# Performance work log

Hardware: AMD Instinct MI355X
Metric: run time of the kernel (lower is better)

The kernel has to match this reference:

```python
import jax, jax.numpy as jnp
import numpy as np

EMBED = 1024
HEADS = 16
HEAD_DIM = EMBED // HEADS


def setup_inputs() -> dict:
    key = jax.random.key(0)
    ks = jax.random.split(key, 7)
    N, L = 2, 2048
    values = jax.random.normal(ks[0], (N, L, EMBED), dtype=jnp.float32)
    keys = jax.random.normal(ks[1], (N, L, EMBED), dtype=jnp.float32)
    queries = jax.random.normal(ks[2], (N, L, EMBED), dtype=jnp.float32)
    mask = jax.random.randint(ks[3], (N, 1, L, L), 0, 2, dtype=jnp.int32)
    s = 1.0 / np.sqrt(HEAD_DIM)
    Wv = jax.random.normal(ks[4], (HEAD_DIM, HEAD_DIM), dtype=jnp.float32) * s
    Wk = jax.random.normal(ks[5], (HEAD_DIM, HEAD_DIM), dtype=jnp.float32) * s
    Wq = jax.random.normal(ks[6], (HEAD_DIM, HEAD_DIM), dtype=jnp.float32) * s
    return {"values": values, "keys": keys, "queries": queries, "mask": mask,
            "Wv": Wv, "Wk": Wk, "Wq": Wq}


def reference(values, keys, queries, mask, Wv, Wk, Wq):
    N, Lq = queries.shape[0], queries.shape[1]
    Lk = keys.shape[1]
    # reshape to [N, L, H, D]; nn.Linear(x) = x @ W.T (shared across heads)
    v = values.reshape(N, Lk, HEADS, HEAD_DIM) @ Wv.T
    k = keys.reshape(N, Lk, HEADS, HEAD_DIM) @ Wk.T
    q = queries.reshape(N, Lq, HEADS, HEAD_DIM) @ Wq.T
    # scores scaled by sqrt(embed_size) as in the original module
    e = jnp.einsum("nqhd,nkhd->nhqk", q, k) / jnp.sqrt(jnp.float32(EMBED))
    e = jnp.where(mask == 0, jnp.float32(-1e20), e)
    attn = jax.nn.softmax(e, axis=-1)
    out = jnp.einsum("nhqk,nkhd->nqhd", attn, v)
    return out.reshape(N, Lq, HEADS * HEAD_DIM)
```

## Files before the change

### kernel.cpp

```cpp
#include <hip/hip_runtime.h>
#include <hip/hip_bf16.h>

#define LSEQ 2048
#define NB   2
#define NH   16
#define HD   64
#define NKT  32
#define QSCALE 0.04508687049285173f

typedef __attribute__((ext_vector_type(8))) __bf16 bf16x8;
typedef __attribute__((ext_vector_type(4))) __bf16 bf16x4;
typedef __attribute__((ext_vector_type(2))) __bf16 bf16x2;
typedef __attribute__((ext_vector_type(4))) float  f32x4;

__global__ __launch_bounds__(256)
void pack_mask_kernel(const int* __restrict__ mask,
                      unsigned long long* __restrict__ mbits) {
  size_t gw = ((size_t)blockIdx.x * 256 + threadIdx.x) >> 6;
  int lane = threadIdx.x & 63;
  int v = mask[gw * 64 + lane];
  unsigned long long b = __ballot(v != 0);
  if (lane == 0) mbits[gw] = b;
}

__global__ __launch_bounds__(256)
void proj_kernel(const float* __restrict__ xv, const float* __restrict__ Wv_,
                 const float* __restrict__ xk, const float* __restrict__ Wk_,
                 const float* __restrict__ xq, const float* __restrict__ Wq_,
                 __bf16* __restrict__ outv, __bf16* __restrict__ outk,
                 __bf16* __restrict__ outq) {
  __shared__ __bf16 S[16384];
  __bf16* Xh = S;
  __bf16* Xl = S + 4096;
  __bf16* Wh = S + 8192;
  __bf16* Wl = S + 12288;

  const float* x; const float* W; __bf16* out;
  if (blockIdx.z == 0)      { x = xv; W = Wv_; out = outv; }
  else if (blockIdx.z == 1) { x = xk; W = Wk_; out = outk; }
  else                      { x = xq; W = Wq_; out = outq; }
  const float osc = (blockIdx.z == 2) ? QSCALE : 1.0f;

  const int tid = threadIdx.x;
  const int bx = blockIdx.x;
  const int h  = blockIdx.y;
  const int n  = bx >> 5;
  const int l0 = (bx & 31) << 6;

  const int r  = tid >> 2;
  const int c0 = (tid & 3) << 4;
  const float* xrow = x + ((size_t)(n * LSEQ + l0) + r) * 1024 + h * 64 + c0;
  const float* wrow = W + r * 64 + c0;

#pragma unroll
  for (int hf = 0; hf < 2; ++hf) {
    int kc = c0 + hf * 8;
    int off = r * 64 + (kc ^ ((r & 7) << 3));
    float4 a = *(const float4*)(xrow + hf * 8);
    float4 b = *(const float4*)(xrow + hf * 8 + 4);
    float va[8] = {a.x, a.y, a.z, a.w, b.x, b.y, b.z, b.w};
    bf16x8 hi, lo;
#pragma unroll
    for (int j = 0; j < 8; ++j) {
      __bf16 h_ = (__bf16)va[j];
      hi[j] = h_;
      lo[j] = (__bf16)(va[j] - (float)h_);
    }
    *(bf16x8*)(Xh + off) = hi;
    *(bf16x8*)(Xl + off) = lo;

    float4 c = *(const float4*)(wrow + hf * 8);
    float4 d = *(const float4*)(wrow + hf * 8 + 4);
    float vw[8] = {c.x, c.y, c.z, c.w, d.x, d.y, d.z, d.w};
    bf16x8 whv, wlv;
#pragma unroll
    for (int j = 0; j < 8; ++j) {
      __bf16 h_ = (__bf16)vw[j];
      whv[j] = h_;
      wlv[j] = (__bf16)(vw[j] - (float)h_);
    }
    *(bf16x8*)(Wh + off) = whv;
    *(bf16x8*)(Wl + off) = wlv;
  }
  __syncthreads();

  const int wv   = tid >> 6;
  const int lane = tid & 63;
  const int l15  = lane & 15;
  const int lhi  = lane >> 4;

  bf16x8 xhf[2], xlf[2];
  const int arow = wv * 16 + l15;
#pragma unroll
  for (int ko = 0; ko < 2; ++ko) {
    int aoff = arow * 64 + ((ko * 32 + lhi * 8) ^ ((arow & 7) << 3));
    xhf[ko] = *(const bf16x8*)(Xh + aoff);
    xlf[ko] = *(const bf16x8*)(Xl + aoff);
  }

  f32x4 acc[4] = {};
#pragma unroll
  for (int cg = 0; cg < 4; ++cg) {
    int d = cg * 16 + l15;
#pragma unroll
    for (int ko = 0; ko < 2; ++ko) {
      int boff = d * 64 + ((ko * 32 + lhi * 8) ^ ((d & 7) << 3));
      bf16x8 whf = *(const bf16x8*)(Wh + boff);
      bf16x8 wlf = *(const bf16x8*)(Wl + boff);
      acc[cg] = __builtin_amdgcn_mfma_f32_16x16x32_bf16(xhf[ko], whf, acc[cg], 0, 0, 0);
      acc[cg] = __builtin_amdgcn_mfma_f32_16x16x32_bf16(xhf[ko], wlf, acc[cg], 0, 0, 0);
      acc[cg] = __builtin_amdgcn_mfma_f32_16x16x32_bf16(xlf[ko], whf, acc[cg], 0, 0, 0);
    }
  }
  __syncthreads();

  __bf16* tb = S;
#pragma unroll
  for (int cg = 0; cg < 4; ++cg)
#pragma unroll
    for (int rr = 0; rr < 4; ++rr)
      tb[(wv * 16 + lhi * 4 + rr) * 72 + cg * 16 + l15] = (__bf16)(acc[cg][rr] * osc);
  __syncthreads();

  const int tok = tid >> 2;
  const int d0  = (tid & 3) * 16;
  bf16x8 o0 = *(const bf16x8*)(tb + tok * 72 + d0);
  bf16x8 o1 = *(const bf16x8*)(tb + tok * 72 + d0 + 8);
  size_t ob = (size_t)(n * NH + h) * LSEQ + l0;
  *(bf16x8*)(out + (ob + tok) * HD + d0)     = o0;
  *(bf16x8*)(out + (ob + tok) * HD + d0 + 8) = o1;
}

__global__ __launch_bounds__(512, 4)
void attn_kernel(const __bf16* __restrict__ Qb, const __bf16* __restrict__ Kb,
                 const __bf16* __restrict__ Vb,
                 const unsigned long long* __restrict__ mbits,
                 float* __restrict__ out) {
  __shared__ __bf16 KV[16384];
  __shared__ float  Ls[128];

  const int tid  = threadIdx.x;
  const int wid  = tid >> 6;
  const int hw   = wid >> 2;
  const int wq   = wid & 3;
  const int lane = tid & 63;
  const int l15  = lane & 15;
  const int lhi  = lane >> 4;

  const int lin = blockIdx.y * 16 + blockIdx.x;
  const int xcd = lin & 7;
  const int idx = lin >> 3;
  const int nh  = xcd + ((idx >> 4) << 3);
  const int qt  = idx & 15;
  const int n   = nh >> 4;
  const int h   = nh & 15;
  const int q0  = qt << 7;

  const __bf16* Qg = Qb + ((size_t)nh * LSEQ + q0) * HD;
  const __bf16* Kg = Kb + (size_t)nh * LSEQ * HD;
  const __bf16* Vg = Vb + (size_t)nh * LSEQ * HD;

  bf16x8 qf[2][2];
#pragma unroll
  for (int mi = 0; mi < 2; ++mi)
#pragma unroll
    for (int ks = 0; ks < 2; ++ks)
      qf[mi][ks] = *(const bf16x8*)(Qg + (size_t)(wq * 32 + mi * 16 + l15) * HD
                                       + ks * 32 + lhi * 8);

  f32x4 o[2][4] = {};
  f32x4 o_ls[2] = {};
  const unsigned long long* mrow0 =
      mbits + ((size_t)n * LSEQ + q0 + wq * 32 + l15) * NKT;
  const unsigned long long* mrow1 = mrow0 + (size_t)16 * NKT;

  bf16x8 onesf;
#pragma unroll
  for (int j = 0; j < 8; ++j) onesf[j] = (__bf16)1.0f;

  const int vkg  = lane & 15;
  const int vdgw = (wq << 2) + lhi;
  const int vslotbase = ((vkg & 8) << 2) + ((vkg & 3) << 3) + (((vkg >> 2) & 1) << 2);
  bf16x4 vv[4];

#define STAGE_K(kt_, buf_)                                                         \
  _Pragma("unroll")                                                                \
  for (int it = 0; it < 2; ++it) {                                                 \
    int chb = wq * 64 + it * 256;                                                  \
    int ch = chb + lane;                                                           \
    int skey = ch >> 3, sdc = ch & 7;                                              \
    const __bf16* src = Kg + (size_t)(kt_) * 4096 + skey * 64 + ((sdc ^ (skey & 7)) << 3); \
    __builtin_amdgcn_global_load_lds(                                              \
        (const __attribute__((address_space(1))) void*)src,                        \
        (__attribute__((address_space(3))) void*)(KV + (buf_) * 4096 + chb * 8), 16, 0, 0); \
  }
#define LOAD_V(kt_)                                                                \
  _Pragma("unroll")                                                                \
  for (int m_ = 0; m_ < 4; ++m_)                                                   \
    vv[m_] = *(const bf16x4*)(Vg + (size_t)(kt_) * 4096 + (vkg * 4 + m_) * HD + vdgw * 4);
#define WRITE_V(buf_)                                                              \
  _Pragma("unroll")                                                                \
  for (int i = 0; i < 4; ++i) {                                                    \
    int d = vdgw * 4 + i;                                                          \
    int swz = (d & 7) ^ ((d >> 3) & 7);                                            \
    bf16x4 pr; pr[0] = vv[0][i]; pr[1] = vv[1][i]; pr[2] = vv[2][i]; pr[3] = vv[3][i]; \
    *(bf16x4*)(KV + 8192 + (buf_) * 4096 + d * 64 + (vslotbase ^ (swz << 3))) = pr; \
  }

  if (hw == 1) { STAGE_K(0, 0); }
  else         { LOAD_V(0); WRITE_V(0); }
  unsigned long long w0 = mrow0[0];
  unsigned long long w1 = mrow1[0];
  __syncthreads();

  for (int kt = 0; kt < NKT; ++kt) {
    const int cur = kt & 1;
    const int nxt = cur ^ 1;
    const bool pf = (kt + 1 < NKT);
    unsigned long long nw0 = 0, nw1 = 0;
    if (pf) {
      if (hw == 1) { STAGE_K(kt + 1, nxt); }
      else         { LOAD_V(kt + 1); }
      nw0 = mrow0[kt + 1];
      nw1 = mrow1[kt + 1];
    }

    const __bf16* Kc = KV + cur * 4096;
    f32x4 s[2][2] = {};
#pragma unroll
    for (int ks = 0; ks < 2; ++ks)
#pragma unroll
      for (int t = 0; t < 2; ++t) {
        int key = hw * 32 + t * 16 + l15;
        bf16x8 kf = *(const bf16x8*)(
            Kc + key * 64 + ((ks * 32 + lhi * 8) ^ ((key & 7) << 3)));
        s[0][t] = __builtin_amdgcn_mfma_f32_16x16x32_bf16(kf, qf[0][ks], s[0][t], 0, 0, 0);
        s[1][t] = __builtin_amdgcn_mfma_f32_16x16x32_bf16(kf, qf[1][ks], s[1][t], 0, 0, 0);
      }

    bf16x8 pa[2];
#pragma unroll
    for (int mi = 0; mi < 2; ++mi) {
      unsigned long long w = mi ? w1 : w0;
      unsigned shl = (unsigned)(w >> (hw * 32 + lhi * 4));
#pragma unroll
      for (int t = 0; t < 2; ++t)
#pragma unroll
        for (int r = 0; r < 4; ++r) {
          float p = __builtin_amdgcn_exp2f(s[mi][t][r]);
          p = ((shl >> (t * 16 + r)) & 1u) ? p : 0.f;
          pa[mi][t * 4 + r] = (__bf16)p;
        }
    }

    if (hw == 0 && pf) { WRITE_V(nxt); }

    const __bf16* Vc = KV + 8192 + cur * 4096;
#pragma unroll
    for (int t = 0; t < 4; ++t) {
      int d = t * 16 + l15;
      int swz = (d & 7) ^ ((d >> 3) & 7);
      bf16x8 vf = *(const bf16x8*)(
          Vc + d * 64 + ((hw * 32 + lhi * 8) ^ (swz << 3)));
      o[0][t] = __builtin_amdgcn_mfma_f32_16x16x32_bf16(pa[0], vf, o[0][t], 0, 0, 0);
      o[1][t] = __builtin_amdgcn_mfma_f32_16x16x32_bf16(pa[1], vf, o[1][t], 0, 0, 0);
    }
    o_ls[0] = __builtin_amdgcn_mfma_f32_16x16x32_bf16(pa[0], onesf, o_ls[0], 0, 0, 0);
    o_ls[1] = __builtin_amdgcn_mfma_f32_16x16x32_bf16(pa[1], onesf, o_ls[1], 0, 0, 0);

    w0 = nw0;
    w1 = nw1;
    __syncthreads();
  }

  float* Sf = (float*)KV;
  if (hw == 1) {
#pragma unroll
    for (int mi = 0; mi < 2; ++mi) {
#pragma unroll
      for (int t = 0; t < 4; ++t)
        *(f32x4*)&Sf[wq * 2048 + (mi * 4 + t) * 256 + lane * 4] = o[mi][t];
      if (l15 == 0)
        *(f32x4*)&Ls[wq * 32 + mi * 16 + lhi * 4] = o_ls[mi];
    }
  }
  __syncthreads();
  if (hw == 0) {
#pragma unroll
    for (int mi = 0; mi < 2; ++mi) {
      f32x4 pls = *(const f32x4*)&Ls[wq * 32 + mi * 16 + lhi * 4];
      float inv[4];
#pragma unroll
      for (int r = 0; r < 4; ++r)
        inv[r] = 1.f / (o_ls[mi][r] + pls[r]);
#pragma unroll
      for (int t = 0; t < 4; ++t) {
        f32x4 po = *(const f32x4*)&Sf[wq * 2048 + (mi * 4 + t) * 256 + lane * 4];
#pragma unroll
        for (int r = 0; r < 4; ++r) {
          size_t ob = ((size_t)n * LSEQ + q0 + wq * 32 + mi * 16 + lhi * 4 + r) * 1024
                    + h * 64 + t * 16 + l15;
          out[ob] = (o[mi][t][r] + po[r]) * inv[r];
        }
      }
    }
  }
#undef STAGE_K
#undef LOAD_V
#undef WRITE_V
}

extern "C" void kernel_launch(void* const* d_in, const int* in_sizes, int n_in,
                              void* d_out, int out_size, void* d_ws, size_t ws_size,
                              hipStream_t stream) {
  const float* xv   = (const float*)d_in[0];
  const float* xk   = (const float*)d_in[1];
  const float* xq   = (const float*)d_in[2];
  const int*   mask = (const int*)d_in[3];
  const float* Wv   = (const float*)d_in[4];
  const float* Wk   = (const float*)d_in[5];
  const float* Wq   = (const float*)d_in[6];
  float* out = (float*)d_out;

  const size_t elems = (size_t)NB * NH * LSEQ * HD;
  __bf16* Qw = (__bf16*)d_ws;
  __bf16* Kw = Qw + elems;
  __bf16* Vw = Kw + elems;
  unsigned long long* mb = (unsigned long long*)(Vw + elems);

  pack_mask_kernel<<<dim3(NB * LSEQ * NKT / 4), 256, 0, stream>>>(mask, mb);
  proj_kernel<<<dim3(64, NH, 3), 256, 0, stream>>>(xv, Wv, xk, Wk, xq, Wq,
                                                   Vw, Kw, Qw);
  attn_kernel<<<dim3(16, 32), 512, 0, stream>>>(Qw, Kw, Vw, mb, out);
}
```

Baseline: 103.1 us.

## Process two key tiles per barrier with four-deep K/V LDS buffering

Restructures the attention main loop so that each synchronization period computes two key tiles and prefetches the next two into a four-slot LDS ring, doubling shared memory for K and V. This halves the number of block-wide barriers and deepens the prefetch distance, which should hide more global-load latency. The cost is twice the LDS use (64KB plus), which may cut occupancy below the launch bound's four blocks per CU, plus extra registers for the second V staging buffer.

Result: slower. 251.0 us (+143.4%).

```diff
diff --git a/kernel.cpp b/kernel.cpp
--- a/kernel.cpp
+++ b/kernel.cpp
@@ -136,7 +136,7 @@
                  const __bf16* __restrict__ Vb,
                  const unsigned long long* __restrict__ mbits,
                  float* __restrict__ out) {
-  __shared__ __bf16 KV[16384];
+  __shared__ __bf16 KV[32768];
   __shared__ float  Ls[128];
 
   const int tid  = threadIdx.x;
@@ -181,7 +181,7 @@
   const int vkg  = lane & 15;
   const int vdgw = (wq << 2) + lhi;
   const int vslotbase = ((vkg & 8) << 2) + ((vkg & 3) << 3) + (((vkg >> 2) & 1) << 2);
-  bf16x4 vv[4];
+  bf16x4 vvA[4], vvB[4];
 
 #define STAGE_K(kt_, buf_)                                                         \
   _Pragma("unroll")                                                                \
@@ -194,83 +194,92 @@
         (const __attribute__((address_space(1))) void*)src,                        \
         (__attribute__((address_space(3))) void*)(KV + (buf_) * 4096 + chb * 8), 16, 0, 0); \
   }
-#define LOAD_V(kt_)                                                                \
+#define LOAD_V(kt_, vv_)                                                           \
   _Pragma("unroll")                                                                \
   for (int m_ = 0; m_ < 4; ++m_)                                                   \
-    vv[m_] = *(const bf16x4*)(Vg + (size_t)(kt_) * 4096 + (vkg * 4 + m_) * HD + vdgw * 4);
-#define WRITE_V(buf_)                                                              \
+    vv_[m_] = *(const bf16x4*)(Vg + (size_t)(kt_) * 4096 + (vkg * 4 + m_) * HD + vdgw * 4);
+#define WRITE_V(buf_, vv_)                                                         \
   _Pragma("unroll")                                                                \
   for (int i = 0; i < 4; ++i) {                                                    \
     int d = vdgw * 4 + i;                                                          \
     int swz = (d & 7) ^ ((d >> 3) & 7);                                            \
-    bf16x4 pr; pr[0] = vv[0][i]; pr[1] = vv[1][i]; pr[2] = vv[2][i]; pr[3] = vv[3][i]; \
-    *(bf16x4*)(KV + 8192 + (buf_) * 4096 + d * 64 + (vslotbase ^ (swz << 3))) = pr; \
-  }
-
-  if (hw == 1) { STAGE_K(0, 0); }
-  else         { LOAD_V(0); WRITE_V(0); }
-  unsigned long long w0 = mrow0[0];
-  unsigned long long w1 = mrow1[0];
-  __syncthreads();
-
-  for (int kt = 0; kt < NKT; ++kt) {
-    const int cur = kt & 1;
-    const int nxt = cur ^ 1;
-    const bool pf = (kt + 1 < NKT);
-    unsigned long long nw0 = 0, nw1 = 0;
-    if (pf) {
-      if (hw == 1) { STAGE_K(kt + 1, nxt); }
-      else         { LOAD_V(kt + 1); }
-      nw0 = mrow0[kt + 1];
-      nw1 = mrow1[kt + 1];
-    }
-
-    const __bf16* Kc = KV + cur * 4096;
-    f32x4 s[2][2] = {};
-#pragma unroll
-    for (int ks = 0; ks < 2; ++ks)
-#pragma unroll
-      for (int t = 0; t < 2; ++t) {
-        int key = hw * 32 + t * 16 + l15;
-        bf16x8 kf = *(const bf16x8*)(
-            Kc + key * 64 + ((ks * 32 + lhi * 8) ^ ((key & 7) << 3)));
-        s[0][t] = __builtin_amdgcn_mfma_f32_16x16x32_bf16(kf, qf[0][ks], s[0][t], 0, 0, 0);
-        s[1][t] = __builtin_amdgcn_mfma_f32_16x16x32_bf16(kf, qf[1][ks], s[1][t], 0, 0, 0);
-      }
-
-    bf16x8 pa[2];
-#pragma unroll
-    for (int mi = 0; mi < 2; ++mi) {
-      unsigned long long w = mi ? w1 : w0;
-      unsigned shl = (unsigned)(w >> (hw * 32 + lhi * 4));
-#pragma unroll
-      for (int t = 0; t < 2; ++t)
-#pragma unroll
-        for (int r = 0; r < 4; ++r) {
-          float p = __builtin_amdgcn_exp2f(s[mi][t][r]);
-          p = ((shl >> (t * 16 + r)) & 1u) ? p : 0.f;
-          pa[mi][t * 4 + r] = (__bf16)p;
-        }
-    }
-
-    if (hw == 0 && pf) { WRITE_V(nxt); }
-
-    const __bf16* Vc = KV + 8192 + cur * 4096;
-#pragma unroll
-    for (int t = 0; t < 4; ++t) {
-      int d = t * 16 + l15;
-      int swz = (d & 7) ^ ((d >> 3) & 7);
-      bf16x8 vf = *(const bf16x8*)(
-          Vc + d * 64 + ((hw * 32 + lhi * 8) ^ (swz << 3)));
-      o[0][t] = __builtin_amdgcn_mfma_f32_16x16x32_bf16(pa[0], vf, o[0][t], 0, 0, 0);
-      o[1][t] = __builtin_amdgcn_mfma_f32_16x16x32_bf16(pa[1], vf, o[1][t], 0, 0, 0);
-    }
-    o_ls[0] = __builtin_amdgcn_mfma_f32_16x16x32_bf16(pa[0], onesf, o_ls[0], 0, 0, 0);
-    o_ls[1] = __builtin_amdgcn_mfma_f32_16x16x32_bf16(pa[1], onesf, o_ls[1], 0, 0, 0);
-
-    w0 = nw0;
-    w1 = nw1;
-    __syncthreads();
+    bf16x4 pr; pr[0] = vv_[0][i]; pr[1] = vv_[1][i]; pr[2] = vv_[2][i]; pr[3] = vv_[3][i]; \
+    *(bf16x4*)(KV + 16384 + (buf_) * 4096 + d * 64 + (vslotbase ^ (swz << 3))) = pr; \
+  }
+
+#define COMPUTE(W0_, W1_, cb_)                                                     \
+  {                                                                                \
+    const __bf16* Kc = KV + (cb_) * 4096;                                          \
+    f32x4 s[2][2] = {};                                                            \
+    _Pragma("unroll")                                                              \
+    for (int ks = 0; ks < 2; ++ks)                                                 \
+      _Pragma("unroll")                                                            \
+      for (int t = 0; t < 2; ++t) {                                                \
+        int key = hw * 32 + t * 16 + l15;                                          \
+        bf16x8 kf = *(const bf16x8*)(                                              \
+            Kc + key * 64 + ((ks * 32 + lhi * 8) ^ ((key & 7) << 3)));             \
+        s[0][t] = __builtin_amdgcn_mfma_f32_16x16x32_bf16(kf, qf[0][ks], s[0][t], 0, 0, 0); \
+        s[1][t] = __builtin_amdgcn_mfma_f32_16x16x32_bf16(kf, qf[1][ks], s[1][t], 0, 0, 0); \
+      }                                                                            \
+    bf16x8 pa[2];                                                                  \
+    _Pragma("unroll")                                                              \
+    for (int mi = 0; mi < 2; ++mi) {                                               \
+      unsigned long long w = mi ? (W1_) : (W0_);                                   \
+      unsigned shl = (unsigned)(w >> (hw * 32 + lhi * 4));                         \
+      _Pragma("unroll")                                                            \
+      for (int t = 0; t < 2; ++t)                                                  \
+        _Pragma("unroll")                                                          \
+        for (int r = 0; r < 4; ++r) {                                              \
+          float p = __builtin_amdgcn_exp2f(s[mi][t][r]);                           \
+          p = ((shl >> (t * 16 + r)) & 1u) ? p : 0.f;                              \
+          pa[mi][t * 4 + r] = (__bf16)p;                                           \
+        }                                                                          \
+    }                                                                              \
+    const __bf16* Vc = KV + 16384 + (cb_) * 4096;                                  \
+    _Pragma("unroll")                                                              \
+    for (int t = 0; t < 4; ++t) {                                                  \
+      int d = t * 16 + l15;                                                        \
+      int swz = (d & 7) ^ ((d >> 3) & 7);                                          \
+      bf16x8 vf = *(const bf16x8*)(                                                \
+          Vc + d * 64 + ((hw * 32 + lhi * 8) ^ (swz << 3)));                       \
+      o[0][t] = __builtin_amdgcn_mfma_f32_16x16x32_bf16(pa[0], vf, o[0][t], 0, 0, 0); \
+      o[1][t] = __builtin_amdgcn_mfma_f32_16x16x32_bf16(pa[1], vf, o[1][t], 0, 0, 0); \
+    }                                                                              \
+    o_ls[0] = __builtin_amdgcn_mfma_f32_16x16x32_bf16(pa[0], onesf, o_ls[0], 0, 0, 0); \
+    o_ls[1] = __builtin_amdgcn_mfma_f32_16x16x32_bf16(pa[1], onesf, o_ls[1], 0, 0, 0); \
+  }
+
+  unsigned long long w0a, w1a, w0b, w1b;
+  unsigned long long nw0a = 0, nw1a = 0, nw0b = 0, nw1b = 0;
+
+  if (hw == 1) { STAGE_K(0, 0); STAGE_K(1, 1); }
+  else         { LOAD_V(0, vvA); LOAD_V(1, vvB); }
+  w0a = mrow0[0]; w1a = mrow1[0];
+  w0b = mrow0[1]; w1b = mrow1[1];
+  if (hw == 0) { WRITE_V(0, vvA); WRITE_V(1, vvB); }
+  __syncthreads();
+
+#define PERIOD(t0_, ca_, cb_, na_, nb_, st_)                                       \
+  {                                                                                \
+    if (st_) {                                                                     \
+      if (hw == 1) { STAGE_K((t0_) + 2, na_); STAGE_K((t0_) + 3, nb_); }           \
+      else         { LOAD_V((t0_) + 2, vvA); LOAD_V((t0_) + 3, vvB); }             \
+      nw0a = mrow0[(t0_) + 2]; nw1a = mrow1[(t0_) + 2];                            \
+      nw0b = mrow0[(t0_) + 3]; nw1b = mrow1[(t0_) + 3];                            \
+    }                                                                              \
+    COMPUTE(w0a, w1a, ca_);                                                        \
+    if ((st_) && hw == 0) { WRITE_V(na_, vvA); }                                   \
+    COMPUTE(w0b, w1b, cb_);                                                        \
+    if ((st_) && hw == 0) { WRITE_V(nb_, vvB); }                                   \
+    w0a = nw0a; w1a = nw1a; w0b = nw0b; w1b = nw1b;                                \
+    __syncthreads();                                                               \
+  }
+
+  for (int kt4 = 0; kt4 < 8; ++kt4) {
+    const int t0 = kt4 * 4;
+    PERIOD(t0, 0, 1, 2, 3, true);
+    if (kt4 < 7) { PERIOD(t0 + 2, 2, 3, 0, 1, true); }
+    else         { PERIOD(t0 + 2, 2, 3, 0, 1, false); }
   }
 
   float* Sf = (float*)KV;
@@ -308,6 +317,8 @@
 #undef STAGE_K
 #undef LOAD_V
 #undef WRITE_V
+#undef COMPUTE
+#undef PERIOD
 }
 
 extern "C" void kernel_launch(void* const* d_in, const int* in_sizes, int n_in,
```
